# Kernel optimization log

Measured on AMD Instinct MI355X. Metric: run time of the kernel, lower is better.

The kernel has to match this reference:

```python
import jax, jax.numpy as jnp
import numpy as np

BSZ, L, H, P = 4, 4096, 1024, 512
DT_MIN, DT_MAX = 1e-3, 1e-1


def setup_inputs() -> dict:
    key = jax.random.key(0)
    ks = jax.random.split(key, 6)
    input_sequence = jax.random.normal(ks[0], (BSZ, 1, H, 1, L), jnp.float32)
    # hidden_state_method='zero': hiddens arg only has to carry the right shape
    hiddens = jnp.zeros((BSZ, 1, P), jnp.float32)
    # stable (left-half-plane) diagonal state matrix, like HiPPO-LegS eigenvalues
    Lambda_re = -0.5 * jax.random.uniform(ks[1], (P,), jnp.float32) - 0.1
    Lambda_im = jnp.pi * jnp.arange(P, dtype=jnp.float32)
    # B stored as (P, H, 2) real/imag pair (lecun-ish scale), C as (H, P, 2)
    B = jax.random.normal(ks[2], (P, H, 2), jnp.float32) / jnp.sqrt(2.0 * H)
    C = jax.random.normal(ks[3], (H, P, 2), jnp.float32) / jnp.sqrt(2.0 * P)
    D = jax.random.normal(ks[4], (H,), jnp.float32)
    log_step = jax.random.uniform(ks[5], (P, 1), jnp.float32,
                                  minval=float(np.log(DT_MIN)),
                                  maxval=float(np.log(DT_MAX)))
    return dict(input_sequence=input_sequence, hiddens=hiddens,
                Lambda_re=Lambda_re, Lambda_im=Lambda_im,
                B=B, C=C, D=D, log_step=log_step)


def _binop(qi, qj):
    # diagonal linear recurrence combine: x_j = A_j * x_i + b_j
    Ai, bi = qi
    Aj, bj = qj
    return (Aj * Ai, Aj * bi + bj)


def _s5_forward(input_sequence, Lambda_re, Lambda_im, B, C, D, log_step):
    Lam = jax.lax.complex(Lambda_re, Lambda_im)              # (P,)
    step = jnp.exp(log_step[:, 0])                           # (P,)
    # zero-order-hold discretization
    Lambda_bar = jnp.exp(Lam * step)                         # (P,) complex
    B_scale = (Lambda_bar - 1.0) / Lam                       # (P,) complex
    B_bar_re = B_scale.real[:, None] * B[..., 0] - B_scale.imag[:, None] * B[..., 1]
    B_bar_im = B_scale.real[:, None] * B[..., 1] + B_scale.imag[:, None] * B[..., 0]

    u = input_sequence[:, 0, :, 0].transpose(0, 2, 1)        # (BSZ, L, H) float32

    # Bu_t = B_bar @ u_t, done on real/imag parts to keep u real in the GEMM
    Bu = jax.lax.complex(jnp.einsum('blh,ph->blp', u, B_bar_re),
                         jnp.einsum('blh,ph->blp', u, B_bar_im))  # (BSZ,L,P)
    # prepend zero hidden state (hidden_state_method='zero')
    zeros0 = jnp.zeros((Bu.shape[0], 1, Bu.shape[2]), Bu.dtype)
    Bu_elems = jnp.concatenate([zeros0, Bu], axis=1)          # (BSZ,L+1,P)
    Lam_elems = jnp.broadcast_to(Lambda_bar, Bu_elems.shape)  # (BSZ,L+1,P)

    _, xs = jax.lax.associative_scan(_binop, (Lam_elems, Bu_elems), axis=1)
    xs = xs[:, 1:]                                            # (BSZ,L,P) complex states

    # conj_sym=True: y_t = 2 * Re(C_tilde @ x_t)
    Cr, Ci = C[..., 0], C[..., 1]                             # (H,P) each
    ys = 2.0 * (jnp.einsum('hp,blp->blh', Cr, xs.real)
                - jnp.einsum('hp,blp->blh', Ci, xs.imag))     # (BSZ,L,H)
    ys = ys + D * u                                           # feedthrough
    ys = jax.nn.gelu(ys, approximate=False)                   # activation='gelu'
    return ys.transpose(0, 2, 1)[:, None, :, None, :]         # (BSZ,1,H,1,L)


def reference(input_sequence, hiddens, Lambda_re, Lambda_im, B, C, D, log_step):
    del hiddens  # unused with hidden_state_method='zero'
    return _s5_forward(input_sequence, Lambda_re, Lambda_im, B, C, D, log_step)
```

## Files before the change

kernel.cpp:

```cpp
#include <hip/hip_runtime.h>
#include <math.h>


constexpr int kB = 4, kL = 4096, kH = 1024, kP = 512;
constexpr int kM = 1024, kK = 1024, kN = 4096;

typedef short bf16x8 __attribute__((ext_vector_type(8)));
typedef float f32x4 __attribute__((ext_vector_type(4)));

constexpr size_t A1H_OFF = 0;
constexpr size_t A2H_OFF = A1H_OFF + (size_t)kM * kK * 2;
constexpr size_t LBAR_B  = A2H_OFF + (size_t)kM * kK * 2;
constexpr size_t BU_B    = (LBAR_B + 4096 + 255) & ~(size_t)255;
constexpr size_t TH_B    = BU_B + (size_t)kB * kM * kN * 4;
constexpr size_t MID_BYTES = TH_B + (size_t)kB * kN * kK * 2;

__device__ __forceinline__ unsigned short f2bf(float x) {
  unsigned int u = __float_as_uint(x);
  u += 0x7fffu + ((u >> 16) & 1u);
  return (unsigned short)(u >> 16);
}
__device__ __forceinline__ float bf2f(unsigned short h) {
  return __uint_as_float(((unsigned int)h) << 16);
}

__device__ __forceinline__ void gl2lds16(const void* g, void* l) {
  __builtin_amdgcn_global_load_lds(
      (const __attribute__((address_space(1))) void*)g,
      (__attribute__((address_space(3))) void*)l, 16, 0, 0);
}

template <int N>
__device__ __forceinline__ void wait_vm() {
  __builtin_amdgcn_s_waitcnt((N & 15) | ((N >> 4) << 14) | (15 << 8) | (7 << 4));
}

__global__ __launch_bounds__(256) void k_prep1(
    const float* __restrict__ Lre, const float* __restrict__ Lim,
    const float* __restrict__ B, const float* __restrict__ log_step,
    unsigned char* __restrict__ ws) {
  int p = blockIdx.x;
  float lr = Lre[p], li = Lim[p];
  float step = expf(log_step[p]);
  float er = expf(lr * step);
  float sb, cb;
  sincosf(li * step, &sb, &cb);
  float lbr = er * cb, lbi = er * sb;
  float nr = lbr - 1.0f, ni = lbi;
  float inv = 1.0f / (lr * lr + li * li);
  float sr = (nr * lr + ni * li) * inv;
  float si = (ni * lr - nr * li) * inv;

  if (threadIdx.x == 0) ((float2*)(ws + LBAR_B))[p] = make_float2(lbr, lbi);

  unsigned short* a1h = (unsigned short*)(ws + A1H_OFF);
  const float* Brow = B + (size_t)p * kH * 2;
  for (int h = threadIdx.x; h < kH; h += 256) {
    float br = Brow[2 * h], bi = Brow[2 * h + 1];
    a1h[(size_t)p * kK + h] = f2bf(sr * br - si * bi);
    a1h[(size_t)(kP + p) * kK + h] = f2bf(sr * bi + si * br);
  }
}

__global__ __launch_bounds__(256) void k_prep2(
    const float* __restrict__ C, unsigned char* __restrict__ ws) {
  int h = blockIdx.x;
  unsigned short* a2h = (unsigned short*)(ws + A2H_OFF);
  for (int k = threadIdx.x; k < kK; k += 256) {
    float v = (k < kP) ? 2.f * C[((size_t)h * kP + k) * 2]
                       : -2.f * C[((size_t)h * kP + (k - kP)) * 2 + 1];
    a2h[(size_t)h * kK + k] = f2bf(v);
  }
}

__global__ __launch_bounds__(256) void k_transpose(
    const float* __restrict__ in, unsigned short* __restrict__ oh) {
  __shared__ float t[64][65];
  int b = blockIdx.z;
  int r0 = blockIdx.y * 64;
  int c0 = blockIdx.x * 64;
  int tid = threadIdx.x;
  const float* src = in + ((size_t)b * 1024 + r0) * 4096 + c0;
  int cc = (tid & 15) * 4, rr = tid >> 4;
#pragma unroll
  for (int i = 0; i < 4; i++) {
    float4 v = *(const float4*)(src + (size_t)(rr + i * 16) * 4096 + cc);
    t[rr + i * 16][cc + 0] = v.x;
    t[rr + i * 16][cc + 1] = v.y;
    t[rr + i * 16][cc + 2] = v.z;
    t[rr + i * 16][cc + 3] = v.w;
  }
  __syncthreads();
  int oc = tid >> 2;
  int og = (tid & 3) * 2;
#pragma unroll
  for (int i = 0; i < 2; i++) {
    int g = og + i;
    unsigned short hv[8];
#pragma unroll
    for (int j = 0; j < 8; j++) hv[j] = f2bf(t[g * 8 + j][oc]);
    size_t ob = ((size_t)b * 4096 + c0 + oc) * 1024 + r0 + g * 8;
    *(uint4*)(oh + ob) = *(uint4*)hv;
  }
}


__device__ __forceinline__ int stage_src_off32(int Dp) {
  int Ds = Dp ^ (((Dp >> 9) & 1) << 5);
  int s = Ds >> 10, d = Ds & 1023;
  int row = (s << 4) + (d >> 6);
  int kk = (d & 63) >> 1;
  return row * kK + kk;
}

template <int MH>
__device__ __forceinline__ void rd_a2(bf16x8 (&a)[2], const unsigned char* lds,
                                      int base, int wmrb, int lane_off) {
#pragma unroll
  for (int i = 0; i < 2; i++)
    a[i] = *(const bf16x8*)(lds + base + ((wmrb + MH * 2 + i) << 10) + lane_off);
}
template <int NH>
__device__ __forceinline__ void rd_b2(bf16x8 (&bb)[2][2], const unsigned char* lds,
                                      int base, int wnrb, int lane_off) {
#pragma unroll
  for (int i = 0; i < 2; i++)
    bb[NH][i] = *(const bf16x8*)(lds + base + ((wnrb + NH * 2 + i) << 10) + lane_off);
}

template <int MH, int NH>
__device__ __forceinline__ void quad4(f32x4 (&acc)[4][4], bf16x8 (&a)[2],
                                      bf16x8 (&bb)[2][2]) {
  __builtin_amdgcn_s_setprio(1);
#pragma unroll
  for (int mi = 0; mi < 2; mi++)
#pragma unroll
    for (int nj = 0; nj < 2; nj++)
      acc[MH * 2 + mi][NH * 2 + nj] = __builtin_amdgcn_mfma_f32_16x16x32_bf16(
          a[mi], bb[NH][nj], acc[MH * 2 + mi][NH * 2 + nj], 0, 0, 0);
  __builtin_amdgcn_s_setprio(0);
}

#define BAR __builtin_amdgcn_s_barrier()
#define LGKM0                                           \
  do {                                                  \
    asm volatile("s_waitcnt lgkmcnt(0)" ::: "memory");  \
    __builtin_amdgcn_sched_barrier(0);                  \
  } while (0)

template <bool EPI>
__global__ __launch_bounds__(512, 4) void k_gemm32(
    const unsigned short* __restrict__ Ah, const unsigned short* __restrict__ Bh,
    float* __restrict__ out, const float* __restrict__ u,
    const float* __restrict__ D) {
  __shared__ __align__(16) unsigned char lds[49152];
  constexpr int LA0 = 0, LA1 = 8192, LB0 = 16384, LB1 = 32768;
  constexpr int NT2 = kK / 64;

  int b = blockIdx.z;
  int m0 = blockIdx.y * 128, n0 = blockIdx.x * 256;
  int tid = threadIdx.x, w = tid >> 6;
  int q = (tid >> 4) & 3, r = tid & 15;
  int wm = (w >> 2) * 64, wn = (w & 3) * 64;
  int wmrb = (w >> 2) * 4, wnrb = (w & 3) * 4;
  int lane_off = (r * 64 + q * 16) ^ ((r & 8) << 2);

  int d0 = tid << 4;
  int rowk = stage_src_off32(d0);

  const unsigned short* pA = Ah + (size_t)m0 * kK;
  const unsigned short* pB = Bh + (size_t)b * kN * kK + (size_t)n0 * kK;

  f32x4 acc[4][4] = {};
  bf16x8 a[2], bb[2][2];

#define STG_A(KT, LB)                                             \
  gl2lds16(pA + (KT) * 32 + rowk, lds + (LB) + d0)
#define STG_B(H, KT, LB)                                          \
  gl2lds16(pB + (size_t)(H) * 128 * kK + (KT) * 32 + rowk,        \
           lds + (LB) + (H) * 8192 + d0)

  STG_A(0, LA0);
  STG_B(0, 0, LB0); STG_B(1, 0, LB0);
  STG_B(0, 1, LB1); STG_B(1, 1, LB1);
  wait_vm<2>();
  BAR;

  for (int it = 0; it < NT2; ++it) {
    int kt = it * 2;
    bool pf = (it + 1 < NT2);
    rd_a2<0>(a, lds, LA0, wmrb, lane_off);
    rd_b2<0>(bb, lds, LB0, wnrb, lane_off);
    STG_A(kt + 1, LA1);
    BAR; LGKM0; quad4<0, 0>(acc, a, bb); BAR;
    rd_b2<1>(bb, lds, LB0, wnrb, lane_off);
    BAR; LGKM0; quad4<0, 1>(acc, a, bb); BAR;
    rd_a2<1>(a, lds, LA0, wmrb, lane_off);
    if (pf) STG_B(0, kt + 2, LB0);
    BAR; LGKM0; quad4<1, 1>(acc, a, bb); BAR;
    if (pf) STG_B(1, kt + 2, LB0);
    BAR; quad4<1, 0>(acc, a, bb);
    if (pf) wait_vm<2>(); else wait_vm<0>();
    BAR;
    rd_a2<0>(a, lds, LA1, wmrb, lane_off);
    rd_b2<0>(bb, lds, LB1, wnrb, lane_off);
    if (pf) STG_A(kt + 2, LA0);
    BAR; LGKM0; quad4<0, 0>(acc, a, bb); BAR;
    rd_b2<1>(bb, lds, LB1, wnrb, lane_off);
    BAR; LGKM0; quad4<0, 1>(acc, a, bb); BAR;
    rd_a2<1>(a, lds, LA1, wmrb, lane_off);
    if (pf) STG_B(0, kt + 3, LB1);
    BAR; LGKM0; quad4<1, 1>(acc, a, bb); BAR;
    if (pf) STG_B(1, kt + 3, LB1);
    BAR; quad4<1, 0>(acc, a, bb);
    if (pf) wait_vm<2>();
    BAR;
  }
#undef STG_A
#undef STG_B

#pragma unroll
  for (int mi = 0; mi < 4; mi++) {
#pragma unroll
    for (int reg = 0; reg < 4; reg++) {
      int row = m0 + wm + mi * 16 + q * 4 + reg;
      float dv = EPI ? D[row] : 0.f;
#pragma unroll
      for (int ni = 0; ni < 4; ni++) {
        int col = n0 + wn + ni * 16 + r;
        size_t o = ((size_t)b * kM + row) * (size_t)kN + col;
        float v = acc[mi][ni][reg];
        if (EPI) {
          float y = v + dv * u[o];
          v = 0.5f * y * (1.f + erff(y * 0.70710678118654752f));
        }
        out[o] = v;
      }
    }
  }
}

__global__ __launch_bounds__(256) void k_scan(float* __restrict__ bu,
                                              const float2* __restrict__ lbar) {
  int p = blockIdx.x & (kP - 1);
  int b = blockIdx.x >> 9;
  int tid = threadIdx.x, lane = tid & 63, w = tid >> 6;
  float2 lam = lbar[p];
  float* sre = bu + ((size_t)b * kM + p) * (size_t)kN;
  float* sim = sre + (size_t)kP * kN;

  float vr[16], vi[16];
  {
    const float4* pr = (const float4*)(sre + tid * 16);
    const float4* pi = (const float4*)(sim + tid * 16);
#pragma unroll
    for (int i = 0; i < 4; i++) {
      float4 a = pr[i], c = pi[i];
      vr[4 * i] = a.x; vr[4 * i + 1] = a.y; vr[4 * i + 2] = a.z; vr[4 * i + 3] = a.w;
      vi[4 * i] = c.x; vi[4 * i + 1] = c.y; vi[4 * i + 2] = c.z; vi[4 * i + 3] = c.w;
    }
  }

  float xr = 0.f, xi = 0.f;
#pragma unroll
  for (int i = 0; i < 16; i++) {
    float nr2 = fmaf(lam.x, xr, fmaf(-lam.y, xi, vr[i]));
    float ni2 = fmaf(lam.x, xi, fmaf(lam.y, xr, vi[i]));
    xr = nr2; xi = ni2;
  }

  float Ar = lam.x, Ai = lam.y;
#pragma unroll
  for (int s = 0; s < 4; s++) {
    float tr = Ar * Ar - Ai * Ai, ti = 2.f * Ar * Ai;
    Ar = tr; Ai = ti;
  }
  float br = xr, bi = xi;

  for (int off = 1; off < 64; off <<= 1) {
    float pAr = __shfl_up(Ar, off), pAi = __shfl_up(Ai, off);
    float pbr = __shfl_up(br, off), pbi = __shfl_up(bi, off);
    if (lane >= off) {
      float nAr = Ar * pAr - Ai * pAi;
      float nAi = Ar * pAi + Ai * pAr;
      float nbr = Ar * pbr - Ai * pbi + br;
      float nbi = Ar * pbi + Ai * pbr + bi;
      Ar = nAr; Ai = nAi; br = nbr; bi = nbi;
    }
  }

  __shared__ float4 wtot[4];
  if (lane == 63) wtot[w] = make_float4(Ar, Ai, br, bi);
  __syncthreads();

  float eAr = __shfl_up(Ar, 1), eAi = __shfl_up(Ai, 1);
  float ebr = __shfl_up(br, 1), ebi = __shfl_up(bi, 1);
  if (lane == 0) { eAr = 1.f; eAi = 0.f; ebr = 0.f; ebi = 0.f; }

  float pAr = 1.f, pAi = 0.f, pbr = 0.f, pbi = 0.f;
  for (int j = 0; j < w; j++) {
    float4 t = wtot[j];
    float nAr = t.x * pAr - t.y * pAi;
    float nAi = t.x * pAi + t.y * pAr;
    float nbr = t.x * pbr - t.y * pbi + t.z;
    float nbi = t.x * pbi + t.y * pbr + t.w;
    pAr = nAr; pAi = nAi; pbr = nbr; pbi = nbi;
  }

  float initr = eAr * pbr - eAi * pbi + ebr;
  float initi = eAr * pbi + eAi * pbr + ebi;

  xr = initr; xi = initi;
  float4* qr = (float4*)(sre + tid * 16);
  float4* qi = (float4*)(sim + tid * 16);
#pragma unroll
  for (int i = 0; i < 4; i++) {
    float rr[4], ii[4];
#pragma unroll
    for (int j = 0; j < 4; j++) {
      float nr2 = fmaf(lam.x, xr, fmaf(-lam.y, xi, vr[4 * i + j]));
      float ni2 = fmaf(lam.x, xi, fmaf(lam.y, xr, vi[4 * i + j]));
      xr = nr2; xi = ni2; rr[j] = nr2; ii[j] = ni2;
    }
    qr[i] = make_float4(rr[0], rr[1], rr[2], rr[3]);
    qi[i] = make_float4(ii[0], ii[1], ii[2], ii[3]);
  }
}

constexpr size_t OBBAR = 0;
constexpr size_t OLBAR = (size_t)kP * kH;
constexpr size_t OBU = OLBAR + 1024;

__global__ __launch_bounds__(256) void k_precomputeF(
    const float* __restrict__ Lre, const float* __restrict__ Lim,
    const float* __restrict__ B, const float* __restrict__ log_step,
    float2* __restrict__ ws) {
  int p = blockIdx.x;
  float lr = Lre[p], li = Lim[p];
  float step = expf(log_step[p]);
  float er = expf(lr * step);
  float sb, cb;
  sincosf(li * step, &sb, &cb);
  float lbr = er * cb, lbi = er * sb;
  float nr = lbr - 1.0f, ni = lbi;
  float inv = 1.0f / (lr * lr + li * li);
  float sr = (nr * lr + ni * li) * inv;
  float si = (ni * lr - nr * li) * inv;
  if (threadIdx.x == 0) ws[OLBAR + p] = make_float2(lbr, lbi);
  float2* Bbar = ws + OBBAR;
  const float* Brow = B + (size_t)p * kH * 2;
  for (int h = threadIdx.x; h < kH; h += 256) {
    float br = Brow[2 * h], bi = Brow[2 * h + 1];
    Bbar[(size_t)p * kH + h] = make_float2(sr * br - si * bi, sr * bi + si * br);
  }
}

__global__ __launch_bounds__(256) void k_gemm1F(
    const float2* __restrict__ ws_bbar, const float* __restrict__ u,
    float2* __restrict__ Bu) {
  __shared__ float2 As[16][64];
  __shared__ float Bs[16][64];
  int b = blockIdx.z, m0 = blockIdx.y * 64, n0 = blockIdx.x * 64;
  int tid = threadIdx.x, tn = tid & 15, tm = tid >> 4;
  const float* uB = u + (size_t)b * kH * kL;
  float2 acc[4][4];
#pragma unroll
  for (int i = 0; i < 4; i++)
#pragma unroll
    for (int j = 0; j < 4; j++) acc[i][j] = make_float2(0.f, 0.f);
  int ar = tid >> 2, ac = (tid & 3) * 4, bk = tid >> 4, bc = (tid & 15) * 4;
  for (int k0 = 0; k0 < kH; k0 += 16) {
    const float4* src = (const float4*)(ws_bbar + (size_t)(m0 + ar) * kH + k0 + ac);
    float4 v01 = src[0], v23 = src[1];
    As[ac + 0][ar] = make_float2(v01.x, v01.y);
    As[ac + 1][ar] = make_float2(v01.z, v01.w);
    As[ac + 2][ar] = make_float2(v23.x, v23.y);
    As[ac + 3][ar] = make_float2(v23.z, v23.w);
    float4 v = *(const float4*)(uB + (size_t)(k0 + bk) * kL + n0 + bc);
    *(float4*)&Bs[bk][bc] = v;
    __syncthreads();
#pragma unroll
    for (int kk = 0; kk < 16; ++kk) {
      const float4* arow = (const float4*)&As[kk][0];
      float4 a01 = arow[tm * 2 + 0], a23 = arow[tm * 2 + 1];
      float2 a[4] = {make_float2(a01.x, a01.y), make_float2(a01.z, a01.w),
                     make_float2(a23.x, a23.y), make_float2(a23.z, a23.w)};
      float4 bv = ((const float4*)&Bs[kk][0])[tn];
      float bbv[4] = {bv.x, bv.y, bv.z, bv.w};
#pragma unroll
      for (int mi = 0; mi < 4; mi++)
#pragma unroll
        for (int ni = 0; ni < 4; ni++) {
          acc[mi][ni].x = fmaf(a[mi].x, bbv[ni], acc[mi][ni].x);
          acc[mi][ni].y = fmaf(a[mi].y, bbv[ni], acc[mi][ni].y);
        }
    }
    __syncthreads();
  }
  float2* BuB = Bu + (size_t)b * kP * kL;
#pragma unroll
  for (int mi = 0; mi < 4; mi++) {
    int row = m0 + tm * 4 + mi;
    float2* dst = BuB + (size_t)row * kL + n0 + tn * 4;
    ((float4*)dst)[0] = make_float4(acc[mi][0].x, acc[mi][0].y, acc[mi][1].x, acc[mi][1].y);
    ((float4*)dst)[1] = make_float4(acc[mi][2].x, acc[mi][2].y, acc[mi][3].x, acc[mi][3].y);
  }
}

__global__ __launch_bounds__(256) void k_scanF(float2* __restrict__ Bu,
                                               const float2* __restrict__ Lbar) {
  int p = blockIdx.x & (kP - 1);
  int b = blockIdx.x >> 9;
  int tid = threadIdx.x, lane = tid & 63, w = tid >> 6;
  float2 lam = Lbar[p];
  float2* seq = Bu + ((size_t)b * kP + p) * kL;
  float2 v[16];
  const float4* src = (const float4*)(seq + tid * 16);
#pragma unroll
  for (int i = 0; i < 8; i++) {
    float4 t = src[i];
    v[2 * i] = make_float2(t.x, t.y);
    v[2 * i + 1] = make_float2(t.z, t.w);
  }
  float xr = 0.f, xi = 0.f;
#pragma unroll
  for (int i = 0; i < 16; i++) {
    float nr2 = fmaf(lam.x, xr, fmaf(-lam.y, xi, v[i].x));
    float ni2 = fmaf(lam.x, xi, fmaf(lam.y, xr, v[i].y));
    xr = nr2; xi = ni2;
  }
  float Ar = lam.x, Ai = lam.y;
#pragma unroll
  for (int s = 0; s < 4; s++) {
    float tr = Ar * Ar - Ai * Ai, ti = 2.f * Ar * Ai;
    Ar = tr; Ai = ti;
  }
  float br = xr, bi = xi;
  for (int off = 1; off < 64; off <<= 1) {
    float pAr = __shfl_up(Ar, off), pAi = __shfl_up(Ai, off);
    float pbr = __shfl_up(br, off), pbi = __shfl_up(bi, off);
    if (lane >= off) {
      float nAr = Ar * pAr - Ai * pAi, nAi = Ar * pAi + Ai * pAr;
      float nbr = Ar * pbr - Ai * pbi + br, nbi = Ar * pbi + Ai * pbr + bi;
      Ar = nAr; Ai = nAi; br = nbr; bi = nbi;
    }
  }
  __shared__ float4 wtot[4];
  if (lane == 63) wtot[w] = make_float4(Ar, Ai, br, bi);
  __syncthreads();
  float eAr = __shfl_up(Ar, 1), eAi = __shfl_up(Ai, 1);
  float ebr = __shfl_up(br, 1), ebi = __shfl_up(bi, 1);
  if (lane == 0) { eAr = 1.f; eAi = 0.f; ebr = 0.f; ebi = 0.f; }
  float pAr = 1.f, pAi = 0.f, pbr = 0.f, pbi = 0.f;
  for (int j = 0; j < w; j++) {
    float4 t = wtot[j];
    float nAr = t.x * pAr - t.y * pAi, nAi = t.x * pAi + t.y * pAr;
    float nbr = t.x * pbr - t.y * pbi + t.z, nbi = t.x * pbi + t.y * pbr + t.w;
    pAr = nAr; pAi = nAi; pbr = nbr; pbi = nbi;
  }
  float initr = eAr * pbr - eAi * pbi + ebr;
  float initi = eAr * pbi + eAi * pbr + ebi;
  xr = initr; xi = initi;
  float4* dst = (float4*)(seq + tid * 16);
#pragma unroll
  for (int i = 0; i < 8; i++) {
    float nr0 = fmaf(lam.x, xr, fmaf(-lam.y, xi, v[2 * i].x));
    float ni0 = fmaf(lam.x, xi, fmaf(lam.y, xr, v[2 * i].y));
    float nr1 = fmaf(lam.x, nr0, fmaf(-lam.y, ni0, v[2 * i + 1].x));
    float ni1 = fmaf(lam.x, ni0, fmaf(lam.y, nr0, v[2 * i + 1].y));
    dst[i] = make_float4(nr0, ni0, nr1, ni1);
    xr = nr1; xi = ni1;
  }
}

__global__ __launch_bounds__(256) void k_gemm2F(
    const float2* __restrict__ C, const float2* __restrict__ X,
    const float* __restrict__ u, const float* __restrict__ D,
    float* __restrict__ out) {
  __shared__ float2 As[16][64];
  __shared__ float2 Bs[16][64];
  int b = blockIdx.z, m0 = blockIdx.y * 64, n0 = blockIdx.x * 64;
  int tid = threadIdx.x, tn = tid & 15, tm = tid >> 4;
  const float2* Xb = X + (size_t)b * kP * kL;
  float acc[4][4];
#pragma unroll
  for (int i = 0; i < 4; i++)
#pragma unroll
    for (int j = 0; j < 4; j++) acc[i][j] = 0.f;
  int ar = tid >> 2, ac = (tid & 3) * 4, bk = tid >> 4, bc = (tid & 15) * 4;
  for (int k0 = 0; k0 < kP; k0 += 16) {
    const float4* src = (const float4*)(C + (size_t)(m0 + ar) * kP + k0 + ac);
    float4 v01 = src[0], v23 = src[1];
    As[ac + 0][ar] = make_float2(v01.x, v01.y);
    As[ac + 1][ar] = make_float2(v01.z, v01.w);
    As[ac + 2][ar] = make_float2(v23.x, v23.y);
    As[ac + 3][ar] = make_float2(v23.z, v23.w);
    const float4* srcb = (const float4*)(Xb + (size_t)(k0 + bk) * kL + n0 + bc);
    ((float4*)&Bs[bk][bc])[0] = srcb[0];
    ((float4*)&Bs[bk][bc])[1] = srcb[1];
    __syncthreads();
#pragma unroll
    for (int kk = 0; kk < 16; ++kk) {
      const float4* arow = (const float4*)&As[kk][0];
      float4 a01 = arow[tm * 2 + 0], a23 = arow[tm * 2 + 1];
      float2 a[4] = {make_float2(a01.x, a01.y), make_float2(a01.z, a01.w),
                     make_float2(a23.x, a23.y), make_float2(a23.z, a23.w)};
      const float4* brow = (const float4*)&Bs[kk][0];
      float4 b01 = brow[tn * 2 + 0], b23 = brow[tn * 2 + 1];
      float2 bbv[4] = {make_float2(b01.x, b01.y), make_float2(b01.z, b01.w),
                       make_float2(b23.x, b23.y), make_float2(b23.z, b23.w)};
#pragma unroll
      for (int mi = 0; mi < 4; mi++)
#pragma unroll
        for (int ni = 0; ni < 4; ni++) {
          acc[mi][ni] = fmaf(a[mi].x, bbv[ni].x, acc[mi][ni]);
          acc[mi][ni] = fmaf(-a[mi].y, bbv[ni].y, acc[mi][ni]);
        }
    }
    __syncthreads();
  }
#pragma unroll
  for (int mi = 0; mi < 4; mi++) {
    int h = m0 + tm * 4 + mi;
    float d = D[h];
    const float* urow = u + ((size_t)b * kH + h) * kL + n0 + tn * 4;
    float4 uv = *(const float4*)urow;
    float uu[4] = {uv.x, uv.y, uv.z, uv.w};
    float res[4];
#pragma unroll
    for (int ni = 0; ni < 4; ni++) {
      float y = 2.f * acc[mi][ni] + d * uu[ni];
      res[ni] = 0.5f * y * (1.f + erff(y * 0.70710678118654752f));
    }
    float* orow = out + ((size_t)b * kH + h) * kL + n0 + tn * 4;
    *(float4*)orow = make_float4(res[0], res[1], res[2], res[3]);
  }
}

extern "C" void kernel_launch(void* const* d_in, const int* in_sizes, int n_in,
                              void* d_out, int out_size, void* d_ws, size_t ws_size,
                              hipStream_t stream) {
  const float* input_sequence = (const float*)d_in[0];
  const float* Lambda_re = (const float*)d_in[2];
  const float* Lambda_im = (const float*)d_in[3];
  const float* B = (const float*)d_in[4];
  const float* C = (const float*)d_in[5];
  const float* D = (const float*)d_in[6];
  const float* log_step = (const float*)d_in[7];
  float* out = (float*)d_out;

  if (ws_size >= MID_BYTES) {
    unsigned char* ws = (unsigned char*)d_ws;
    unsigned short* a1h = (unsigned short*)(ws + A1H_OFF);
    unsigned short* a2h = (unsigned short*)(ws + A2H_OFF);
    float2* lbar = (float2*)(ws + LBAR_B);
    float* bu = (float*)(ws + BU_B);
    unsigned short* th = (unsigned short*)(ws + TH_B);

    k_prep1<<<dim3(kP), 256, 0, stream>>>(Lambda_re, Lambda_im, B, log_step, ws);
    k_prep2<<<dim3(kH), 256, 0, stream>>>(C, ws);

    dim3 tgrid(kL / 64, 1024 / 64, kB);
    dim3 ggrid(kN / 256, kM / 128, kB);

    k_transpose<<<tgrid, 256, 0, stream>>>(input_sequence, th);
    k_gemm32<false><<<ggrid, 512, 0, stream>>>(a1h, th, bu, nullptr, nullptr);
    k_scan<<<dim3(kB * kP), 256, 0, stream>>>(bu, lbar);
    k_transpose<<<tgrid, 256, 0, stream>>>(bu, th);
    k_gemm32<true><<<ggrid, 512, 0, stream>>>(a2h, th, out, input_sequence, D);
  } else {
    float2* ws = (float2*)d_ws;
    float2* Bbar = ws + OBBAR;
    float2* Lbar = ws + OLBAR;
    float2* Bu = ws + OBU;
    k_precomputeF<<<dim3(kP), 256, 0, stream>>>(Lambda_re, Lambda_im, B, log_step, ws);
    k_gemm1F<<<dim3(kL / 64, kP / 64, kB), 256, 0, stream>>>(Bbar, input_sequence, Bu);
    k_scanF<<<dim3(kB * kP), 256, 0, stream>>>(Bu, Lbar);
    k_gemm2F<<<dim3(kL / 64, kH / 64, kB), 256, 0, stream>>>(
        (const float2*)C, (const float2*)Bu, input_sequence, D, out);
  }
}
```

Baseline: 291.1 us.

## Simplify GEMM to double-buffered full-tile pipeline and merge prep kernels

After: 279.1 us. 4.1% less time.

```diff
diff --git a/kernel.cpp b/kernel.cpp
--- a/kernel.cpp
+++ b/kernel.cpp
@@ -35,41 +35,41 @@
   __builtin_amdgcn_s_waitcnt((N & 15) | ((N >> 4) << 14) | (15 << 8) | (7 << 4));
 }
 
-__global__ __launch_bounds__(256) void k_prep1(
+__global__ __launch_bounds__(256) void k_prep12(
     const float* __restrict__ Lre, const float* __restrict__ Lim,
     const float* __restrict__ B, const float* __restrict__ log_step,
-    unsigned char* __restrict__ ws) {
-  int p = blockIdx.x;
-  float lr = Lre[p], li = Lim[p];
-  float step = expf(log_step[p]);
-  float er = expf(lr * step);
-  float sb, cb;
-  sincosf(li * step, &sb, &cb);
-  float lbr = er * cb, lbi = er * sb;
-  float nr = lbr - 1.0f, ni = lbi;
-  float inv = 1.0f / (lr * lr + li * li);
-  float sr = (nr * lr + ni * li) * inv;
-  float si = (ni * lr - nr * li) * inv;
-
-  if (threadIdx.x == 0) ((float2*)(ws + LBAR_B))[p] = make_float2(lbr, lbi);
-
-  unsigned short* a1h = (unsigned short*)(ws + A1H_OFF);
-  const float* Brow = B + (size_t)p * kH * 2;
-  for (int h = threadIdx.x; h < kH; h += 256) {
-    float br = Brow[2 * h], bi = Brow[2 * h + 1];
-    a1h[(size_t)p * kK + h] = f2bf(sr * br - si * bi);
-    a1h[(size_t)(kP + p) * kK + h] = f2bf(sr * bi + si * br);
-  }
-}
-
-__global__ __launch_bounds__(256) void k_prep2(
     const float* __restrict__ C, unsigned char* __restrict__ ws) {
-  int h = blockIdx.x;
-  unsigned short* a2h = (unsigned short*)(ws + A2H_OFF);
-  for (int k = threadIdx.x; k < kK; k += 256) {
-    float v = (k < kP) ? 2.f * C[((size_t)h * kP + k) * 2]
-                       : -2.f * C[((size_t)h * kP + (k - kP)) * 2 + 1];
-    a2h[(size_t)h * kK + k] = f2bf(v);
+  int bid = blockIdx.x;
+  if (bid < kP) {
+    int p = bid;
+    float lr = Lre[p], li = Lim[p];
+    float step = expf(log_step[p]);
+    float er = expf(lr * step);
+    float sb, cb;
+    sincosf(li * step, &sb, &cb);
+    float lbr = er * cb, lbi = er * sb;
+    float nr = lbr - 1.0f, ni = lbi;
+    float inv = 1.0f / (lr * lr + li * li);
+    float sr = (nr * lr + ni * li) * inv;
+    float si = (ni * lr - nr * li) * inv;
+
+    if (threadIdx.x == 0) ((float2*)(ws + LBAR_B))[p] = make_float2(lbr, lbi);
+
+    unsigned short* a1h = (unsigned short*)(ws + A1H_OFF);
+    const float* Brow = B + (size_t)p * kH * 2;
+    for (int h = threadIdx.x; h < kH; h += 256) {
+      float br = Brow[2 * h], bi = Brow[2 * h + 1];
+      a1h[(size_t)p * kK + h] = f2bf(sr * br - si * bi);
+      a1h[(size_t)(kP + p) * kK + h] = f2bf(sr * bi + si * br);
+    }
+  } else {
+    int h = bid - kP;
+    unsigned short* a2h = (unsigned short*)(ws + A2H_OFF);
+    for (int k = threadIdx.x; k < kK; k += 256) {
+      float v = (k < kP) ? 2.f * C[((size_t)h * kP + k) * 2]
+                         : -2.f * C[((size_t)h * kP + (k - kP)) * 2 + 1];
+      a2h[(size_t)h * kK + k] = f2bf(v);
+    }
   }
 }
 
@@ -113,34 +113,6 @@
   return row * kK + kk;
 }
 
-template <int MH>
-__device__ __forceinline__ void rd_a2(bf16x8 (&a)[2], const unsigned char* lds,
-                                      int base, int wmrb, int lane_off) {
-#pragma unroll
-  for (int i = 0; i < 2; i++)
-    a[i] = *(const bf16x8*)(lds + base + ((wmrb + MH * 2 + i) << 10) + lane_off);
-}
-template <int NH>
-__device__ __forceinline__ void rd_b2(bf16x8 (&bb)[2][2], const unsigned char* lds,
-                                      int base, int wnrb, int lane_off) {
-#pragma unroll
-  for (int i = 0; i < 2; i++)
-    bb[NH][i] = *(const bf16x8*)(lds + base + ((wnrb + NH * 2 + i) << 10) + lane_off);
-}
-
-template <int MH, int NH>
-__device__ __forceinline__ void quad4(f32x4 (&acc)[4][4], bf16x8 (&a)[2],
-                                      bf16x8 (&bb)[2][2]) {
-  __builtin_amdgcn_s_setprio(1);
-#pragma unroll
-  for (int mi = 0; mi < 2; mi++)
-#pragma unroll
-    for (int nj = 0; nj < 2; nj++)
-      acc[MH * 2 + mi][NH * 2 + nj] = __builtin_amdgcn_mfma_f32_16x16x32_bf16(
-          a[mi], bb[NH][nj], acc[MH * 2 + mi][NH * 2 + nj], 0, 0, 0);
-  __builtin_amdgcn_s_setprio(0);
-}
-
 #define BAR __builtin_amdgcn_s_barrier()
 #define LGKM0                                           \
   do {                                                  \
@@ -149,13 +121,13 @@
   } while (0)
 
 template <bool EPI>
-__global__ __launch_bounds__(512, 4) void k_gemm32(
+__global__ __launch_bounds__(512, 4) void k_gemm2p(
     const unsigned short* __restrict__ Ah, const unsigned short* __restrict__ Bh,
     float* __restrict__ out, const float* __restrict__ u,
     const float* __restrict__ D) {
   __shared__ __align__(16) unsigned char lds[49152];
-  constexpr int LA0 = 0, LA1 = 8192, LB0 = 16384, LB1 = 32768;
-  constexpr int NT2 = kK / 64;
+  constexpr int BUF = 24576;
+  constexpr int NKT = kK / 32;
 
   int b = blockIdx.z;
   int m0 = blockIdx.y * 128, n0 = blockIdx.x * 256;
@@ -172,52 +144,53 @@
   const unsigned short* pB = Bh + (size_t)b * kN * kK + (size_t)n0 * kK;
 
   f32x4 acc[4][4] = {};
-  bf16x8 a[2], bb[2][2];
-
-#define STG_A(KT, LB)                                             \
-  gl2lds16(pA + (KT) * 32 + rowk, lds + (LB) + d0)
-#define STG_B(H, KT, LB)                                          \
-  gl2lds16(pB + (size_t)(H) * 128 * kK + (KT) * 32 + rowk,        \
-           lds + (LB) + (H) * 8192 + d0)
-
-  STG_A(0, LA0);
-  STG_B(0, 0, LB0); STG_B(1, 0, LB0);
-  STG_B(0, 1, LB1); STG_B(1, 1, LB1);
-  wait_vm<2>();
+
+#define STG(KT, LB)                                                       \
+  do {                                                                    \
+    gl2lds16(pA + (KT) * 32 + rowk, lds + (LB) + d0);                     \
+    gl2lds16(pB + (KT) * 32 + rowk, lds + (LB) + 8192 + d0);              \
+    gl2lds16(pB + (size_t)128 * kK + (KT) * 32 + rowk,                    \
+             lds + (LB) + 16384 + d0);                                    \
+  } while (0)
+
+#define COMPUTE(LB)                                                       \
+  do {                                                                    \
+    bf16x8 a[4], bb[4];                                                   \
+    _Pragma("unroll")                                                     \
+    for (int mi = 0; mi < 4; mi++)                                        \
+      a[mi] = *(const bf16x8*)(lds + (LB) + ((wmrb + mi) << 10) + lane_off); \
+    _Pragma("unroll")                                                     \
+    for (int nj = 0; nj < 4; nj++)                                        \
+      bb[nj] = *(const bf16x8*)(lds + (LB) + 8192 +                       \
+                                ((wnrb + nj) << 10) + lane_off);          \
+    LGKM0;                                                                \
+    __builtin_amdgcn_s_setprio(1);                                        \
+    _Pragma("unroll")                                                     \
+    for (int mi = 0; mi < 4; mi++)                                        \
+      _Pragma("unroll")                                                   \
+      for (int nj = 0; nj < 4; nj++)                                      \
+        acc[mi][nj] = __builtin_amdgcn_mfma_f32_16x16x32_bf16(            \
+            a[mi], bb[nj], acc[mi][nj], 0, 0, 0);                         \
+    __builtin_amdgcn_s_setprio(0);                                        \
+  } while (0)
+
+  STG(0, 0);
+  wait_vm<0>();
   BAR;
 
-  for (int it = 0; it < NT2; ++it) {
+  for (int it = 0; it < NKT / 2; ++it) {
     int kt = it * 2;
-    bool pf = (it + 1 < NT2);
-    rd_a2<0>(a, lds, LA0, wmrb, lane_off);
-    rd_b2<0>(bb, lds, LB0, wnrb, lane_off);
-    STG_A(kt + 1, LA1);
-    BAR; LGKM0; quad4<0, 0>(acc, a, bb); BAR;
-    rd_b2<1>(bb, lds, LB0, wnrb, lane_off);
-    BAR; LGKM0; quad4<0, 1>(acc, a, bb); BAR;
-    rd_a2<1>(a, lds, LA0, wmrb, lane_off);
-    if (pf) STG_B(0, kt + 2, LB0);
-    BAR; LGKM0; quad4<1, 1>(acc, a, bb); BAR;
-    if (pf) STG_B(1, kt + 2, LB0);
-    BAR; quad4<1, 0>(acc, a, bb);
-    if (pf) wait_vm<2>(); else wait_vm<0>();
+    if (kt + 1 < NKT) STG(kt + 1, BUF);
+    COMPUTE(0);
+    wait_vm<0>();
     BAR;
-    rd_a2<0>(a, lds, LA1, wmrb, lane_off);
-    rd_b2<0>(bb, lds, LB1, wnrb, lane_off);
-    if (pf) STG_A(kt + 2, LA0);
-    BAR; LGKM0; quad4<0, 0>(acc, a, bb); BAR;
-    rd_b2<1>(bb, lds, LB1, wnrb, lane_off);
-    BAR; LGKM0; quad4<0, 1>(acc, a, bb); BAR;
-    rd_a2<1>(a, lds, LA1, wmrb, lane_off);
-    if (pf) STG_B(0, kt + 3, LB1);
-    BAR; LGKM0; quad4<1, 1>(acc, a, bb); BAR;
-    if (pf) STG_B(1, kt + 3, LB1);
-    BAR; quad4<1, 0>(acc, a, bb);
-    if (pf) wait_vm<2>();
+    if (kt + 2 < NKT) STG(kt + 2, 0);
+    COMPUTE(BUF);
+    wait_vm<0>();
     BAR;
   }
-#undef STG_A
-#undef STG_B
+#undef STG
+#undef COMPUTE
 
 #pragma unroll
   for (int mi = 0; mi < 4; mi++) {
@@ -557,17 +530,17 @@
     float* bu = (float*)(ws + BU_B);
     unsigned short* th = (unsigned short*)(ws + TH_B);
 
-    k_prep1<<<dim3(kP), 256, 0, stream>>>(Lambda_re, Lambda_im, B, log_step, ws);
-    k_prep2<<<dim3(kH), 256, 0, stream>>>(C, ws);
+    k_prep12<<<dim3(kP + kH), 256, 0, stream>>>(Lambda_re, Lambda_im, B,
+                                                log_step, C, ws);
 
     dim3 tgrid(kL / 64, 1024 / 64, kB);
     dim3 ggrid(kN / 256, kM / 128, kB);
 
     k_transpose<<<tgrid, 256, 0, stream>>>(input_sequence, th);
-    k_gemm32<false><<<ggrid, 512, 0, stream>>>(a1h, th, bu, nullptr, nullptr);
+    k_gemm2p<false><<<ggrid, 512, 0, stream>>>(a1h, th, bu, nullptr, nullptr);
     k_scan<<<dim3(kB * kP), 256, 0, stream>>>(bu, lbar);
     k_transpose<<<tgrid, 256, 0, stream>>>(bu, th);
-    k_gemm32<true><<<ggrid, 512, 0, stream>>>(a2h, th, out, input_sequence, D);
+    k_gemm2p<true><<<ggrid, 512, 0, stream>>>(a2h, th, out, input_sequence, D);
   } else {
     float2* ws = (float2*)d_ws;
     float2* Bbar = ws + OBBAR;
```
